# Performance work log

Hardware: AMD Instinct MI355X
Metric: run time of the kernel (lower is better)

The kernel has to match this reference:

```python
import jax, jax.numpy as jnp
import numpy as np

B, S, HID = 2, 2048, 768
H, DH = 12, 64
WINDOW = 128
THETA = 10000.0
NEG_INF = -1e9  # keras MHA uses -1e9 additive mask


def _rope(x, theta=THETA):
    """Apply rotary embedding. x: [B, S, H, DH] (rotate over last dim)."""
    s, d = x.shape[1], x.shape[-1]
    inv_freq = 1.0 / (theta ** (jnp.arange(0, d, 2, dtype=jnp.float32) / d))  # [d/2]
    ang = jnp.arange(s, dtype=jnp.float32)[:, None] * inv_freq[None, :]       # [S, d/2]
    cos = jnp.concatenate([jnp.cos(ang), jnp.cos(ang)], axis=-1)[None, :, None, :]  # [1,S,1,d]
    sin = jnp.concatenate([jnp.sin(ang), jnp.sin(ang)], axis=-1)[None, :, None, :]
    x1, x2 = x[..., : d // 2], x[..., d // 2 :]
    rot = jnp.concatenate([-x2, x1], axis=-1)
    return x * cos + rot * sin


def setup_inputs() -> dict:
    key = jax.random.key(0)
    ks = jax.random.split(key, 9)
    std = 0.02
    hidden_states = jax.random.normal(ks[0], (B, S, HID), dtype=jnp.float32)
    attention_mask = jnp.ones((B, S), dtype=jnp.int32)
    Wq = std * jax.random.truncated_normal(ks[1], -2.0, 2.0, (HID, H, DH), dtype=jnp.float32)
    Wk = std * jax.random.truncated_normal(ks[2], -2.0, 2.0, (HID, H, DH), dtype=jnp.float32)
    Wv = std * jax.random.truncated_normal(ks[3], -2.0, 2.0, (HID, H, DH), dtype=jnp.float32)
    Wo = std * jax.random.truncated_normal(ks[4], -2.0, 2.0, (H, DH, HID), dtype=jnp.float32)
    bq = jnp.zeros((H, DH), dtype=jnp.float32)
    bk = jnp.zeros((H, DH), dtype=jnp.float32)
    bv = jnp.zeros((H, DH), dtype=jnp.float32)
    bo = jnp.zeros((HID,), dtype=jnp.float32)
    return {"hidden_states": hidden_states, "attention_mask": attention_mask,
            "Wq": Wq, "bq": bq, "Wk": Wk, "bk": bk, "Wv": Wv, "bv": bv, "Wo": Wo, "bo": bo}


def reference(hidden_states, attention_mask, Wq, bq, Wk, bk, Wv, bv, Wo, bo):
    b, s, _ = hidden_states.shape
    # RoPE applied to raw hidden states split into heads (as in source), then flattened back
    x4 = hidden_states.reshape(b, s, H, DH)
    q_in = _rope(x4).reshape(b, s, HID)
    k_in = _rope(x4).reshape(b, s, HID)
    v_in = hidden_states
    # keras MultiHeadAttention projections
    q = jnp.einsum("bsi,ihd->bshd", q_in, Wq) + bq
    k = jnp.einsum("bsi,ihd->bshd", k_in, Wk) + bk
    v = jnp.einsum("bsi,ihd->bshd", v_in, Wv) + bv
    q = q * (1.0 / jnp.sqrt(jnp.float32(DH)))
    scores = jnp.einsum("bqhd,bkhd->bhqk", q, k)  # [B,H,S,S]
    # combined mask: padding [B,1,1,S] AND sliding window [S,S]
    pad = attention_mask.astype(bool)[:, None, None, :]
    pos = jnp.arange(s, dtype=jnp.int32)
    win = (jnp.abs(pos[:, None] - pos[None, :]) < WINDOW)[None, None, :, :]
    mask = jnp.logical_and(pad, win)
    scores = scores + (1.0 - mask.astype(scores.dtype)) * NEG_INF
    attn = jax.nn.softmax(scores, axis=-1)
    out = jnp.einsum("bhqk,bkhd->bqhd", attn, v)
    return jnp.einsum("bqhd,hdi->bqi", out, Wo) + bo
```

## Files before the change

### kernel.cpp

```cpp
#include <hip/hip_runtime.h>
#include <hip/hip_bf16.h>
#include <math.h>

#define NB 2
#define NS 2048
#define NHID 768
#define NH 12
#define NDH 64
#define NWIN 128

typedef __attribute__((ext_vector_type(8))) short bf16x8;
typedef __attribute__((ext_vector_type(4))) float f32x4;

__device__ inline unsigned short f2b(float f) {
    union { float f; unsigned int i; } x; x.f = f;
    unsigned int r = x.i + 0x7FFFu + ((x.i >> 16) & 1u);
    return (unsigned short)(r >> 16);
}
__device__ inline int xcd_remap(int flat, int nwg) {
    return (flat & 7) * (nwg >> 3) + (flat >> 3);
}
__device__ __forceinline__ void gload_lds16(const void* g, void* l) {
    __builtin_amdgcn_global_load_lds((const __attribute__((address_space(1))) void*)g,
                                     (__attribute__((address_space(3))) void*)l, 16, 0, 0);
}

__global__ void k_rope_table(float* __restrict__ ct, float* __restrict__ st) {
    int idx = blockIdx.x * 256 + threadIdx.x;
    if (idx >= NS * 32) return;
    int s = idx >> 5, f = idx & 31;
    double inv = pow(10000.0, -((double)(2 * f)) / 64.0);
    double ang = (double)s * inv;
    ct[idx] = (float)cos(ang);
    st[idx] = (float)sin(ang);
}

__global__ void k_rope(const float* __restrict__ x, const float* __restrict__ ct,
                       const float* __restrict__ st, __hip_bfloat16* __restrict__ r,
                       __hip_bfloat16* __restrict__ xb) {
    int idx = blockIdx.x * 256 + threadIdx.x;
    if (idx >= NB * NS * NH * 32) return;
    int f = idx & 31;
    int h = (idx >> 5) % NH;
    int bs = idx / (32 * NH);
    int s = bs & (NS - 1);
    int base = bs * NHID + h * NDH;
    float x1 = x[base + f], x2 = x[base + 32 + f];
    float c = ct[(s << 5) + f], sn = st[(s << 5) + f];
    ((unsigned short*)r)[base + f]      = f2b(x1 * c - x2 * sn);
    ((unsigned short*)r)[base + 32 + f] = f2b(x2 * c + x1 * sn);
    ((unsigned short*)xb)[base + f]      = f2b(x1);
    ((unsigned short*)xb)[base + 32 + f] = f2b(x2);
}

__global__ __launch_bounds__(256) void k_convT(const float* __restrict__ w0, const float* __restrict__ w1,
                                               const float* __restrict__ w2, const float* __restrict__ w3,
                                               __hip_bfloat16* o0, __hip_bfloat16* o1,
                                               __hip_bfloat16* o2, __hip_bfloat16* o3) {
    const float* W; __hip_bfloat16* O;
    switch (blockIdx.z) {
        case 0: W = w0; O = o0; break;
        case 1: W = w1; O = o1; break;
        case 2: W = w2; O = o2; break;
        default: W = w3; O = o3; break;
    }
    __shared__ float tile[64][65];
    int k0 = blockIdx.x * 64, n0 = blockIdx.y * 64;
    int t = threadIdx.x;
    int rr = t >> 4, cc = (t & 15) * 4;
#pragma unroll
    for (int u = 0; u < 4; ++u) {
        int row = rr + u * 16;
        float4 f = *(const float4*)(W + (size_t)(k0 + row) * NHID + n0 + cc);
        tile[row][cc] = f.x; tile[row][cc + 1] = f.y;
        tile[row][cc + 2] = f.z; tile[row][cc + 3] = f.w;
    }
    __syncthreads();
#pragma unroll
    for (int u = 0; u < 4; ++u) {
        int n = rr + u * 16;
        ushort4 s = { f2b(tile[cc + 0][n]), f2b(tile[cc + 1][n]),
                      f2b(tile[cc + 2][n]), f2b(tile[cc + 3][n]) };
        *(ushort4*)((unsigned short*)O + (size_t)(n0 + n) * NHID + k0 + cc) = s;
    }
}

union Frag { bf16x8 v; unsigned long long q[2]; uint4 u; };

template<int MF>
__device__ __forceinline__ void gemm_body(const __hip_bfloat16* __restrict__ A,
                                          const __hip_bfloat16* __restrict__ Wt,
                                          const float* __restrict__ bias,
                                          __hip_bfloat16* __restrict__ Cb,
                                          float* __restrict__ Cf, float scale,
                                          int m0, int n0) {
    constexpr int BM = 32 * MF;
    __shared__ __attribute__((aligned(16))) unsigned short As[BM][64];
    __shared__ __attribute__((aligned(16))) unsigned short Bs[64][64];
    const int t = threadIdx.x;
    const int wid = t >> 6, lane = t & 63;
    const int wm = (wid >> 1) * 16 * MF, wn = (wid & 1) * 32;
    const int g = lane >> 4, r16 = lane & 15;
    const int swz = r16 & 7;

    f32x4 acc[MF][2];
#pragma unroll
    for (int i = 0; i < MF; ++i)
#pragma unroll
        for (int j = 0; j < 2; ++j) acc[i][j] = (f32x4){0.f, 0.f, 0.f, 0.f};

    const int srow = t >> 3;
    const int gslot = (t & 7) ^ (srow & 7);
    const unsigned short* gA = (const unsigned short*)A + (size_t)(m0 + srow) * NHID + gslot * 8;
    const unsigned short* gB = (const unsigned short*)Wt + (size_t)(n0 + srow) * NHID + gslot * 8;
    char* lA = (char*)&As[0][0] + wid * 1024;
    char* lB = (char*)&Bs[0][0] + wid * 1024;

    for (int ks = 0; ks < NHID / 64; ++ks) {
        __syncthreads();
#pragma unroll
        for (int c = 0; c < MF; ++c)
            gload_lds16(gA + (size_t)c * 32 * NHID + ks * 64, lA + c * 4096);
#pragma unroll
        for (int c = 0; c < 2; ++c)
            gload_lds16(gB + (size_t)c * 32 * NHID + ks * 64, lB + c * 4096);
        __syncthreads();
#pragma unroll
        for (int kk = 0; kk < 2; ++kk) {
            Frag af[MF], bf[2];
#pragma unroll
            for (int mi = 0; mi < MF; ++mi)
                af[mi].u = *(const uint4*)&As[wm + mi * 16 + r16][((kk * 4 + g) ^ swz) * 8];
#pragma unroll
            for (int ni = 0; ni < 2; ++ni)
                bf[ni].u = *(const uint4*)&Bs[wn + ni * 16 + r16][((kk * 4 + g) ^ swz) * 8];
#pragma unroll
            for (int mi = 0; mi < MF; ++mi)
#pragma unroll
                for (int ni = 0; ni < 2; ++ni)
                    acc[mi][ni] = __builtin_amdgcn_mfma_f32_16x16x32_bf16(af[mi].v, bf[ni].v, acc[mi][ni], 0, 0, 0);
        }
    }

#pragma unroll
    for (int mi = 0; mi < MF; ++mi)
#pragma unroll
        for (int ni = 0; ni < 2; ++ni)
#pragma unroll
            for (int r = 0; r < 4; ++r) {
                int m = m0 + wm + mi * 16 + 4 * g + r;
                int n = n0 + wn + ni * 16 + r16;
                float v = (acc[mi][ni][r] + bias[n]) * scale;
                if (Cb) ((unsigned short*)Cb)[(size_t)m * NHID + n] = f2b(v);
                else    Cf[(size_t)m * NHID + n] = v;
            }
}

__global__ __launch_bounds__(256) void k_gemm_qkv(const __hip_bfloat16* __restrict__ rb,
                                                  const __hip_bfloat16* __restrict__ xb,
                                                  const __hip_bfloat16* __restrict__ WtQ,
                                                  const __hip_bfloat16* __restrict__ WtK,
                                                  const __hip_bfloat16* __restrict__ WtV,
                                                  const float* __restrict__ bq,
                                                  const float* __restrict__ bk,
                                                  const float* __restrict__ bv,
                                                  __hip_bfloat16* qb, __hip_bfloat16* kb,
                                                  __hip_bfloat16* vb) {
    int flat = blockIdx.x + 12 * blockIdx.y + 384 * blockIdx.z;
    int id = xcd_remap(flat, 1152);
    int z = id / 384, rem = id - z * 384;
    int ty = rem / 12, tx = rem - ty * 12;
    const __hip_bfloat16 *A, *W; const float* bias; __hip_bfloat16* C; float scale;
    switch (z) {
        case 0:  A = rb; W = WtQ; bias = bq; C = qb; scale = 0.125f; break;
        case 1:  A = rb; W = WtK; bias = bk; C = kb; scale = 1.0f;   break;
        default: A = xb; W = WtV; bias = bv; C = vb; scale = 1.0f;   break;
    }
    gemm_body<4>(A, W, bias, C, nullptr, scale, ty * 128, tx * 64);
}

__global__ __launch_bounds__(256) void k_gemm_out(const __hip_bfloat16* __restrict__ A,
                                                  const __hip_bfloat16* __restrict__ Wt,
                                                  const float* __restrict__ bias,
                                                  float* __restrict__ Cf) {
    int flat = blockIdx.x + 12 * blockIdx.y;
    int id = xcd_remap(flat, 768);
    int ty = id / 12, tx = id - ty * 12;
    gemm_body<2>(A, Wt, bias, nullptr, Cf, 1.0f, ty * 64, tx * 64);
}

__global__ __launch_bounds__(256) void k_attn(const __hip_bfloat16* __restrict__ q,
                                              const __hip_bfloat16* __restrict__ kmat,
                                              const __hip_bfloat16* __restrict__ vmat,
                                              const int* __restrict__ am,
                                              __hip_bfloat16* __restrict__ o) {
    __shared__ unsigned short Ks[64][72];
    __shared__ unsigned short Vt[64][72];
    __shared__ float kmask[64];
    const int t = threadIdx.x;
    const int h = blockIdx.y, b = blockIdx.z;
    const int i0 = blockIdx.x * 64;
    const int w = t >> 6, lane = t & 63;
    const int g = lane >> 4, r16 = lane & 15;
    const int qrow = i0 + w * 16 + r16;

    Frag qf[2];
    {
        const unsigned short* qp = (const unsigned short*)q + ((size_t)(b * NS) + qrow) * NHID + h * NDH;
        qf[0].q[0] = *(const unsigned long long*)(qp + 4 * g);
        qf[0].q[1] = *(const unsigned long long*)(qp + 16 + 4 * g);
        qf[1].q[0] = *(const unsigned long long*)(qp + 32 + 4 * g);
        qf[1].q[1] = *(const unsigned long long*)(qp + 48 + 4 * g);
    }
    float m_run = -1e30f, l_run = 0.f;
    f32x4 oacc[4];
#pragma unroll
    for (int i = 0; i < 4; ++i) oacc[i] = (f32x4){0.f, 0.f, 0.f, 0.f};

    for (int kt = 0; kt < 5; ++kt) {
        const int j0 = i0 - 128 + kt * 64;
        if (j0 < 0 || j0 >= NS) continue;
        {
            int key = t >> 2, p = t & 3;
            const unsigned short* kp = (const unsigned short*)kmat +
                ((size_t)(b * NS) + j0 + key) * NHID + h * NDH + p * 16;
            uint4 u0 = *(const uint4*)kp;
            uint4 u1 = *(const uint4*)(kp + 8);
            *(uint4*)&Ks[key][p * 16]     = u0;
            *(uint4*)&Ks[key][p * 16 + 8] = u1;
        }
        {
            int kp2 = t & 31, c = t >> 5;
            const unsigned short* vp = (const unsigned short*)vmat +
                ((size_t)(b * NS) + j0 + 2 * kp2) * NHID + h * NDH + c * 8;
            uint4 v0 = *(const uint4*)vp;
            uint4 v1 = *(const uint4*)(vp + NHID);
            union { uint4 u; unsigned short s[8]; } a0, a1;
            a0.u = v0; a1.u = v1;
#pragma unroll
            for (int e = 0; e < 8; ++e) {
                unsigned int pk = (unsigned int)a0.s[e] | ((unsigned int)a1.s[e] << 16);
                *(unsigned int*)&Vt[c * 8 + e][2 * kp2] = pk;
            }
        }
        if (t < 64) kmask[t] = (am[b * NS + j0 + t] != 0) ? 0.f : -1e30f;
        __syncthreads();

        f32x4 sacc[4];
#pragma unroll
        for (int i = 0; i < 4; ++i) sacc[i] = (f32x4){0.f, 0.f, 0.f, 0.f};
#pragma unroll
        for (int mi = 0; mi < 4; ++mi) {
            Frag kf0, kf1;
            const unsigned short* pk = &Ks[mi * 16 + r16][0];
            kf0.q[0] = *(const unsigned long long*)(pk + 4 * g);
            kf0.q[1] = *(const unsigned long long*)(pk + 16 + 4 * g);
            kf1.q[0] = *(const unsigned long long*)(pk + 32 + 4 * g);
            kf1.q[1] = *(const unsigned long long*)(pk + 48 + 4 * g);
            sacc[mi] = __builtin_amdgcn_mfma_f32_16x16x32_bf16(kf0.v, qf[0].v, sacc[mi], 0, 0, 0);
            sacc[mi] = __builtin_amdgcn_mfma_f32_16x16x32_bf16(kf1.v, qf[1].v, sacc[mi], 0, 0, 0);
        }

        float p[4][4];
        float tmax = -1e30f;
#pragma unroll
        for (int mi = 0; mi < 4; ++mi)
#pragma unroll
            for (int r = 0; r < 4; ++r) {
                int key = j0 + mi * 16 + 4 * g + r;
                float s = sacc[mi][r] + kmask[mi * 16 + 4 * g + r];
                int d = qrow - key; d = d < 0 ? -d : d;
                if (d >= NWIN) s = -1e30f;
                p[mi][r] = s;
                tmax = fmaxf(tmax, s);
            }
        tmax = fmaxf(tmax, __shfl_xor(tmax, 16));
        tmax = fmaxf(tmax, __shfl_xor(tmax, 32));
        float mnew = fmaxf(m_run, tmax);
        float psum = 0.f;
#pragma unroll
        for (int mi = 0; mi < 4; ++mi)
#pragma unroll
            for (int r = 0; r < 4; ++r) {
                float pv = __expf(p[mi][r] - mnew);
                p[mi][r] = pv;
                psum += pv;
            }
        psum += __shfl_xor(psum, 16);
        psum += __shfl_xor(psum, 32);
        float alpha = __expf(m_run - mnew);
        m_run = mnew;
        l_run = l_run * alpha + psum;
#pragma unroll
        for (int mi = 0; mi < 4; ++mi)
#pragma unroll
            for (int r = 0; r < 4; ++r) oacc[mi][r] *= alpha;

        Frag pf[2];
#pragma unroll
        for (int ks2 = 0; ks2 < 2; ++ks2) {
            union { bf16x8 v; unsigned short s[8]; } pp;
#pragma unroll
            for (int r = 0; r < 4; ++r) {
                pp.s[r]     = f2b(p[2 * ks2][r]);
                pp.s[r + 4] = f2b(p[2 * ks2 + 1][r]);
            }
            pf[ks2].v = pp.v;
        }

#pragma unroll
        for (int mi = 0; mi < 4; ++mi) {
            Frag vf0, vf1;
            const unsigned short* pv = &Vt[mi * 16 + r16][0];
            vf0.q[0] = *(const unsigned long long*)(pv + 4 * g);
            vf0.q[1] = *(const unsigned long long*)(pv + 16 + 4 * g);
            vf1.q[0] = *(const unsigned long long*)(pv + 32 + 4 * g);
            vf1.q[1] = *(const unsigned long long*)(pv + 48 + 4 * g);
            oacc[mi] = __builtin_amdgcn_mfma_f32_16x16x32_bf16(vf0.v, pf[0].v, oacc[mi], 0, 0, 0);
            oacc[mi] = __builtin_amdgcn_mfma_f32_16x16x32_bf16(vf1.v, pf[1].v, oacc[mi], 0, 0, 0);
        }
        __syncthreads();
    }

    float inv_l = 1.0f / l_run;
    unsigned short* op = (unsigned short*)o + ((size_t)(b * NS) + qrow) * NHID + h * NDH;
#pragma unroll
    for (int mi = 0; mi < 4; ++mi) {
        ushort4 s = { f2b(oacc[mi][0] * inv_l), f2b(oacc[mi][1] * inv_l),
                      f2b(oacc[mi][2] * inv_l), f2b(oacc[mi][3] * inv_l) };
        *(ushort4*)(op + mi * 16 + 4 * g) = s;
    }
}

extern "C" void kernel_launch(void* const* d_in, const int* in_sizes, int n_in,
                              void* d_out, int out_size, void* d_ws, size_t ws_size,
                              hipStream_t stream) {
    (void)in_sizes; (void)n_in; (void)out_size; (void)ws_size;
    const float* x  = (const float*)d_in[0];
    const int*   am = (const int*)d_in[1];
    const float* Wq = (const float*)d_in[2];
    const float* bq = (const float*)d_in[3];
    const float* Wk = (const float*)d_in[4];
    const float* bk = (const float*)d_in[5];
    const float* Wv = (const float*)d_in[6];
    const float* bv = (const float*)d_in[7];
    const float* Wo = (const float*)d_in[8];
    const float* bo = (const float*)d_in[9];
    float* out = (float*)d_out;
    float* ws  = (float*)d_ws;

    float* ct = ws;
    float* st = ws + 65536;
    __hip_bfloat16* rb  = (__hip_bfloat16*)(ws + 131072);
    __hip_bfloat16* xb  = (__hip_bfloat16*)(ws + 1703936);
    __hip_bfloat16* WtQ = (__hip_bfloat16*)(ws + 3276800);
    __hip_bfloat16* WtK = (__hip_bfloat16*)(ws + 3571712);
    __hip_bfloat16* WtV = (__hip_bfloat16*)(ws + 3866624);
    __hip_bfloat16* WtO = (__hip_bfloat16*)(ws + 4161536);
    __hip_bfloat16* qb  = (__hip_bfloat16*)(ws + 4456448);
    __hip_bfloat16* kb  = (__hip_bfloat16*)(ws + 6029312);
    __hip_bfloat16* vb  = (__hip_bfloat16*)(ws + 7602176);
    __hip_bfloat16* aob = (__hip_bfloat16*)(ws + 9175040);

    k_rope_table<<<256, 256, 0, stream>>>(ct, st);
    k_rope<<<(NB * NS * NH * 32 + 255) / 256, 256, 0, stream>>>(x, ct, st, rb, xb);
    dim3 gt(12, 12, 4);
    k_convT<<<gt, 256, 0, stream>>>(Wq, Wk, Wv, Wo, WtQ, WtK, WtV, WtO);
    dim3 gq(NHID / 64, NB * NS / 128, 3);
    k_gemm_qkv<<<gq, 256, 0, stream>>>(rb, xb, WtQ, WtK, WtV, bq, bk, bv, qb, kb, vb);
    dim3 ga(NS / 64, NH, NB);
    k_attn<<<ga, 256, 0, stream>>>(qb, kb, vb, am, aob);
    dim3 gg(NHID / 64, NB * NS / 64);
    k_gemm_out<<<gg, 256, 0, stream>>>(aob, WtO, bo, out);
}
```

Before: 71.20 us.

## Fuse RoPE table, RoPE, and weight transpose into one prep kernel; prefetch K/V in attention

Replaces three prep launches (double-precision RoPE table, RoPE apply, weight transpose) with one kernel that transposes the weights in some blocks and applies RoPE in the others, computing cos and sin inline in fp32. In attention, the loop bounds are now computed up front instead of skipping out-of-range tiles, and the next K/V tile is loaded into registers while the current tile is being processed, with raw barriers in place of __syncthreads. This removes launch overhead and the table round trip and overlaps global loads with compute. The cost is more register pressure and a small precision difference from fp32 sin/cos at large angles.

```diff
diff --git a/kernel.cpp b/kernel.cpp
--- a/kernel.cpp
+++ b/kernel.cpp
@@ -25,63 +25,58 @@
                                      (__attribute__((address_space(3))) void*)l, 16, 0, 0);
 }
 
-__global__ void k_rope_table(float* __restrict__ ct, float* __restrict__ st) {
-    int idx = blockIdx.x * 256 + threadIdx.x;
-    if (idx >= NS * 32) return;
-    int s = idx >> 5, f = idx & 31;
-    double inv = pow(10000.0, -((double)(2 * f)) / 64.0);
-    double ang = (double)s * inv;
-    ct[idx] = (float)cos(ang);
-    st[idx] = (float)sin(ang);
-}
-
-__global__ void k_rope(const float* __restrict__ x, const float* __restrict__ ct,
-                       const float* __restrict__ st, __hip_bfloat16* __restrict__ r,
-                       __hip_bfloat16* __restrict__ xb) {
-    int idx = blockIdx.x * 256 + threadIdx.x;
-    if (idx >= NB * NS * NH * 32) return;
-    int f = idx & 31;
-    int h = (idx >> 5) % NH;
-    int bs = idx / (32 * NH);
-    int s = bs & (NS - 1);
-    int base = bs * NHID + h * NDH;
-    float x1 = x[base + f], x2 = x[base + 32 + f];
-    float c = ct[(s << 5) + f], sn = st[(s << 5) + f];
-    ((unsigned short*)r)[base + f]      = f2b(x1 * c - x2 * sn);
-    ((unsigned short*)r)[base + 32 + f] = f2b(x2 * c + x1 * sn);
-    ((unsigned short*)xb)[base + f]      = f2b(x1);
-    ((unsigned short*)xb)[base + 32 + f] = f2b(x2);
-}
-
-__global__ __launch_bounds__(256) void k_convT(const float* __restrict__ w0, const float* __restrict__ w1,
-                                               const float* __restrict__ w2, const float* __restrict__ w3,
-                                               __hip_bfloat16* o0, __hip_bfloat16* o1,
-                                               __hip_bfloat16* o2, __hip_bfloat16* o3) {
-    const float* W; __hip_bfloat16* O;
-    switch (blockIdx.z) {
-        case 0: W = w0; O = o0; break;
-        case 1: W = w1; O = o1; break;
-        case 2: W = w2; O = o2; break;
-        default: W = w3; O = o3; break;
-    }
-    __shared__ float tile[64][65];
-    int k0 = blockIdx.x * 64, n0 = blockIdx.y * 64;
+__global__ __launch_bounds__(256) void k_prep(const float* __restrict__ x,
+                                              __hip_bfloat16* __restrict__ rb,
+                                              __hip_bfloat16* __restrict__ xb,
+                                              const float* __restrict__ w0, const float* __restrict__ w1,
+                                              const float* __restrict__ w2, const float* __restrict__ w3,
+                                              __hip_bfloat16* o0, __hip_bfloat16* o1,
+                                              __hip_bfloat16* o2, __hip_bfloat16* o3) {
+    int bid = blockIdx.x;
     int t = threadIdx.x;
-    int rr = t >> 4, cc = (t & 15) * 4;
-#pragma unroll
-    for (int u = 0; u < 4; ++u) {
-        int row = rr + u * 16;
-        float4 f = *(const float4*)(W + (size_t)(k0 + row) * NHID + n0 + cc);
-        tile[row][cc] = f.x; tile[row][cc + 1] = f.y;
-        tile[row][cc + 2] = f.z; tile[row][cc + 3] = f.w;
-    }
-    __syncthreads();
-#pragma unroll
-    for (int u = 0; u < 4; ++u) {
-        int n = rr + u * 16;
-        ushort4 s = { f2b(tile[cc + 0][n]), f2b(tile[cc + 1][n]),
-                      f2b(tile[cc + 2][n]), f2b(tile[cc + 3][n]) };
-        *(ushort4*)((unsigned short*)O + (size_t)(n0 + n) * NHID + k0 + cc) = s;
+    if (bid < 576) {
+        int wsel = bid / 144, r = bid % 144;
+        int kx = r % 12, ny = r / 12;
+        const float* W; __hip_bfloat16* O;
+        switch (wsel) {
+            case 0: W = w0; O = o0; break;
+            case 1: W = w1; O = o1; break;
+            case 2: W = w2; O = o2; break;
+            default: W = w3; O = o3; break;
+        }
+        __shared__ float tile[64][65];
+        int k0 = kx * 64, n0 = ny * 64;
+        int rr = t >> 4, cc = (t & 15) * 4;
+#pragma unroll
+        for (int u = 0; u < 4; ++u) {
+            int row = rr + u * 16;
+            float4 f = *(const float4*)(W + (size_t)(k0 + row) * NHID + n0 + cc);
+            tile[row][cc] = f.x; tile[row][cc + 1] = f.y;
+            tile[row][cc + 2] = f.z; tile[row][cc + 3] = f.w;
+        }
+        __syncthreads();
+#pragma unroll
+        for (int u = 0; u < 4; ++u) {
+            int n = rr + u * 16;
+            ushort4 s = { f2b(tile[cc + 0][n]), f2b(tile[cc + 1][n]),
+                          f2b(tile[cc + 2][n]), f2b(tile[cc + 3][n]) };
+            *(ushort4*)((unsigned short*)O + (size_t)(n0 + n) * NHID + k0 + cc) = s;
+        }
+    } else {
+        int idx = (bid - 576) * 256 + t;
+        int f = idx & 31;
+        int h = (idx >> 5) % NH;
+        int bs = idx / (32 * NH);
+        int s = bs & (NS - 1);
+        int base = bs * NHID + h * NDH;
+        float x1 = x[base + f], x2 = x[base + 32 + f];
+        float inv = exp2f(-0.4152410118609203f * (float)f);
+        float ang = (float)s * inv;
+        float c = cosf(ang), sn = sinf(ang);
+        ((unsigned short*)rb)[base + f]      = f2b(x1 * c - x2 * sn);
+        ((unsigned short*)rb)[base + 32 + f] = f2b(x2 * c + x1 * sn);
+        ((unsigned short*)xb)[base + f]      = f2b(x1);
+        ((unsigned short*)xb)[base + 32 + f] = f2b(x2);
     }
 }
 
@@ -217,34 +212,42 @@
 #pragma unroll
     for (int i = 0; i < 4; ++i) oacc[i] = (f32x4){0.f, 0.f, 0.f, 0.f};
 
-    for (int kt = 0; kt < 5; ++kt) {
+    const int ktL = (i0 == 0) ? 2 : (i0 == 64) ? 1 : 0;
+    const int ktH = (i0 == NS - 64) ? 2 : (i0 == NS - 128) ? 3 : 4;
+
+    uint4 pK0, pK1, pV0, pV1; float pm = 0.f;
+
+#define LOADREGS(KT) do {                                                        \
+    int j0_ = i0 - 128 + (KT) * 64;                                              \
+    const unsigned short* kp_ = (const unsigned short*)kmat +                    \
+        ((size_t)(b * NS) + j0_ + (t >> 2)) * NHID + h * NDH + (t & 3) * 16;     \
+    pK0 = *(const uint4*)kp_;                                                    \
+    pK1 = *(const uint4*)(kp_ + 8);                                              \
+    const unsigned short* vp_ = (const unsigned short*)vmat +                    \
+        ((size_t)(b * NS) + j0_ + 2 * (t & 31)) * NHID + h * NDH + (t >> 5) * 8; \
+    pV0 = *(const uint4*)vp_;                                                    \
+    pV1 = *(const uint4*)(vp_ + NHID);                                           \
+    if (t < 64) pm = (am[b * NS + j0_ + t] != 0) ? 0.f : -1e30f;                 \
+} while (0)
+
+    LOADREGS(ktL);
+    for (int kt = ktL; kt <= ktH; ++kt) {
         const int j0 = i0 - 128 + kt * 64;
-        if (j0 < 0 || j0 >= NS) continue;
         {
-            int key = t >> 2, p = t & 3;
-            const unsigned short* kp = (const unsigned short*)kmat +
-                ((size_t)(b * NS) + j0 + key) * NHID + h * NDH + p * 16;
-            uint4 u0 = *(const uint4*)kp;
-            uint4 u1 = *(const uint4*)(kp + 8);
-            *(uint4*)&Ks[key][p * 16]     = u0;
-            *(uint4*)&Ks[key][p * 16 + 8] = u1;
-        }
-        {
-            int kp2 = t & 31, c = t >> 5;
-            const unsigned short* vp = (const unsigned short*)vmat +
-                ((size_t)(b * NS) + j0 + 2 * kp2) * NHID + h * NDH + c * 8;
-            uint4 v0 = *(const uint4*)vp;
-            uint4 v1 = *(const uint4*)(vp + NHID);
+            *(uint4*)&Ks[t >> 2][(t & 3) * 16]     = pK0;
+            *(uint4*)&Ks[t >> 2][(t & 3) * 16 + 8] = pK1;
             union { uint4 u; unsigned short s[8]; } a0, a1;
-            a0.u = v0; a1.u = v1;
+            a0.u = pV0; a1.u = pV1;
 #pragma unroll
             for (int e = 0; e < 8; ++e) {
                 unsigned int pk = (unsigned int)a0.s[e] | ((unsigned int)a1.s[e] << 16);
-                *(unsigned int*)&Vt[c * 8 + e][2 * kp2] = pk;
-            }
-        }
-        if (t < 64) kmask[t] = (am[b * NS + j0 + t] != 0) ? 0.f : -1e30f;
-        __syncthreads();
+                *(unsigned int*)&Vt[(t >> 5) * 8 + e][2 * (t & 31)] = pk;
+            }
+            if (t < 64) kmask[t] = pm;
+        }
+        if (kt < ktH) LOADREGS(kt + 1);
+        asm volatile("s_waitcnt lgkmcnt(0)" ::: "memory");
+        __builtin_amdgcn_s_barrier();
 
         f32x4 sacc[4];
 #pragma unroll
@@ -319,8 +322,10 @@
             oacc[mi] = __builtin_amdgcn_mfma_f32_16x16x32_bf16(vf0.v, pf[0].v, oacc[mi], 0, 0, 0);
             oacc[mi] = __builtin_amdgcn_mfma_f32_16x16x32_bf16(vf1.v, pf[1].v, oacc[mi], 0, 0, 0);
         }
-        __syncthreads();
-    }
+        asm volatile("s_waitcnt lgkmcnt(0)" ::: "memory");
+        __builtin_amdgcn_s_barrier();
+    }
+#undef LOADREGS
 
     float inv_l = 1.0f / l_run;
     unsigned short* op = (unsigned short*)o + ((size_t)(b * NS) + qrow) * NHID + h * NDH;
@@ -349,23 +354,18 @@
     float* out = (float*)d_out;
     float* ws  = (float*)d_ws;
 
-    float* ct = ws;
-    float* st = ws + 65536;
-    __hip_bfloat16* rb  = (__hip_bfloat16*)(ws + 131072);
-    __hip_bfloat16* xb  = (__hip_bfloat16*)(ws + 1703936);
-    __hip_bfloat16* WtQ = (__hip_bfloat16*)(ws + 3276800);
-    __hip_bfloat16* WtK = (__hip_bfloat16*)(ws + 3571712);
-    __hip_bfloat16* WtV = (__hip_bfloat16*)(ws + 3866624);
-    __hip_bfloat16* WtO = (__hip_bfloat16*)(ws + 4161536);
-    __hip_bfloat16* qb  = (__hip_bfloat16*)(ws + 4456448);
-    __hip_bfloat16* kb  = (__hip_bfloat16*)(ws + 6029312);
-    __hip_bfloat16* vb  = (__hip_bfloat16*)(ws + 7602176);
-    __hip_bfloat16* aob = (__hip_bfloat16*)(ws + 9175040);
-
-    k_rope_table<<<256, 256, 0, stream>>>(ct, st);
-    k_rope<<<(NB * NS * NH * 32 + 255) / 256, 256, 0, stream>>>(x, ct, st, rb, xb);
-    dim3 gt(12, 12, 4);
-    k_convT<<<gt, 256, 0, stream>>>(Wq, Wk, Wv, Wo, WtQ, WtK, WtV, WtO);
+    __hip_bfloat16* rb  = (__hip_bfloat16*)(ws);
+    __hip_bfloat16* xb  = (__hip_bfloat16*)(ws + 1572864);
+    __hip_bfloat16* WtQ = (__hip_bfloat16*)(ws + 3145728);
+    __hip_bfloat16* WtK = (__hip_bfloat16*)(ws + 3440640);
+    __hip_bfloat16* WtV = (__hip_bfloat16*)(ws + 3735552);
+    __hip_bfloat16* WtO = (__hip_bfloat16*)(ws + 4030464);
+    __hip_bfloat16* qb  = (__hip_bfloat16*)(ws + 4325376);
+    __hip_bfloat16* kb  = (__hip_bfloat16*)(ws + 5898240);
+    __hip_bfloat16* vb  = (__hip_bfloat16*)(ws + 7471104);
+    __hip_bfloat16* aob = (__hip_bfloat16*)(ws + 9043968);
+
+    k_prep<<<576 + 6144, 256, 0, stream>>>(x, rb, xb, Wq, Wk, Wv, Wo, WtQ, WtK, WtV, WtO);
     dim3 gq(NHID / 64, NB * NS / 128, 3);
     k_gemm_qkv<<<gq, 256, 0, stream>>>(rb, xb, WtQ, WtK, WtV, bq, bk, bv, qb, kb, vb);
     dim3 ga(NS / 64, NH, NB);
```

After: 64.51 us. 9.4% less time.
